# Kernel tuning notes

Hardware: AMD Instinct MI355X
Metric: run time of the kernel (lower is better)

Reference implementation:

```python
import jax, jax.numpy as jnp
import numpy as np

MAX_Z = 54  # atomic numbers up to iodine (53)
_mv = np.full(MAX_Z, 4.0, np.float32)
for z, v in {6: 4, 7: 3, 8: 2, 16: 6, 9: 1, 17: 1, 35: 1, 53: 1, 15: 5, 1: 1}.items():
    _mv[z] = v
_vdw = np.full(MAX_Z, 1.6, np.float32)  # default_radius = 1.6
for z, r in {1: 1.2, 6: 1.7, 7: 1.55, 8: 1.52, 9: 1.47, 15: 1.8, 16: 1.8, 17: 1.75, 35: 1.85, 53: 1.98}.items():
    _vdw[z] = r
_bl = np.full((MAX_Z, MAX_Z), 1.5, np.float32)  # default_length = 1.5
for (a, b), L in {(6, 6): 1.54, (6, 7): 1.47, (6, 8): 1.43, (6, 16): 1.82, (6, 9): 1.35, (6, 17): 1.77, (6, 1): 1.09, (7, 7): 1.45, (7, 8): 1.40, (7, 1): 1.01, (8, 8): 1.48, (8, 1): 0.96, (16, 16): 2.05, (15, 8): 1.63}.items():
    _bl[a, b] = L
    _bl[b, a] = L  # symmetric == tuple(sorted(...)) lookup
MAX_VAL = jnp.asarray(_mv)
VDW = jnp.asarray(_vdw)
BOND = jnp.asarray(_bl)
BIG = 1e9  # stands in for torch's float('inf') diagonal mask


def _forward(pos, edge_index, atom_types):
    N = pos.shape[0]
    row, col = edge_index[0], edge_index[1]
    # --- valence violations: scatter-add out-degree per atom ---
    bond_counts = jnp.zeros((N,), pos.dtype).at[row].add(1.0)
    violation = jnp.maximum(bond_counts - MAX_VAL[atom_types], 0.0)  # >0 iff counts > max_val
    loss = jnp.sum(violation ** 2)
    # Sequential valence push. Original loops atoms in ascending order and each atom's
    # neighbors in edge-list order; a stable sort of edges by row reproduces exactly that
    # visitation order, so a scan over sorted edges matches the sequential semantics
    # (pos_new[i] updates feed later direction computations).
    order = jnp.argsort(row)  # jnp.argsort is stable
    rs, cs = row[order], col[order]

    def step(p, rc):
        r, c = rc
        v = violation[r]
        d = p[r] - p[c]
        dist = jnp.linalg.norm(d) + 1e-8
        return p.at[r].add(jnp.where(v > 0, d / dist * v * 1e-3, 0.0)), None

    pos_new, _ = jax.lax.scan(step, pos, (rs, cs))
    # --- bond-length correction (gather per edge, scatter back per atom) ---
    bond_vec = pos_new[row] - pos_new[col]                        # [E,3]
    cur_len = jnp.linalg.norm(bond_vec, axis=-1, keepdims=True)   # [E,1]
    tgt_len = BOND[atom_types[row], atom_types[col]][:, None]     # [E,1]
    loss = loss + jnp.mean(jnp.abs(cur_len - tgt_len) ** 2)
    ratio = jnp.clip(tgt_len / (cur_len + 1e-8), 0.98, 1.02)
    adj = (bond_vec * ratio - bond_vec) * 0.01
    pos_new = pos_new + jnp.zeros_like(pos).at[row].add(adj * 0.5).at[col].add(-adj * 0.5)
    # --- steric clash repulsion over all atom pairs (cdist) ---
    sq = jnp.sum(pos_new ** 2, axis=-1)
    d2 = sq[:, None] + sq[None, :] - 2.0 * (pos_new @ pos_new.T)  # [N,N]
    eye = jnp.eye(N, dtype=bool)
    dist = jnp.sqrt(jnp.maximum(jnp.where(eye, 1.0, d2), 1e-20))
    dist = jnp.where(eye, BIG, dist)  # diagonal masked to +inf in the original
    rad = VDW[atom_types]
    min_d = (rad[:, None] + rad[None, :]) * 0.8
    loss = loss + jnp.sum(jax.nn.relu(min_d - dist) ** 2) / 2.0
    # original loops unordered clash pairs i<j updating i and j symmetrically; the full
    # symmetric double sum below is mathematically identical and avoids an [N,N,3] tensor:
    mask = (dist < min_d) & (dist > 1e-8)
    coeff = jnp.where(mask, (min_d - dist) * 0.005 * 0.5 / dist, 0.0)  # [N,N]
    steric = coeff.sum(axis=1)[:, None] * pos_new - coeff @ pos_new    # sum_j c_ij (p_i - p_j)
    return pos_new + steric, loss * 0.1


def setup_inputs() -> dict:
    key = jax.random.key(0)
    k1, k2, k3, k4 = jax.random.split(key, 4)
    N, E = 8192, 32768
    pos = jax.random.normal(k1, (N, 3), jnp.float32) * 6.0  # coords in an ~Angstrom-scale blob
    elements = jnp.array([1, 6, 7, 8, 9, 15, 16, 17], jnp.int32)  # H C N O F P S Cl
    atom_types = elements[jax.random.randint(k2, (N,), 0, 8)]
    edge_index = jnp.stack([jax.random.randint(k3, (E,), 0, N),
                            jax.random.randint(k4, (E,), 0, N)]).astype(jnp.int32)
    return {"pos": pos, "edge_index": edge_index, "atom_types": atom_types}


def reference(pos, edge_index, atom_types):
    return _forward(pos, edge_index, atom_types)
```

## Files before the change

kernel.cpp:

```cpp
#include <hip/hip_runtime.h>
#include <math.h>

#define NA 8192
#define NE 32768
#define NT 256
#define JSPLIT 32
#define JCHUNK (NA / JSPLIT)
#define NIB 16

#define WS_DEG      0
#define WS_LOSS     (WS_DEG + NA)
#define WS_DD       (WS_LOSS + 4)
#define WS_ZERO_END (WS_DD + 3*NA)
#define WS_PART     ((WS_ZERO_END + 3) & ~3)

__device__ __forceinline__ float maxval_of(int z) {
    switch (z) {
        case 1: return 1.f; case 6: return 4.f; case 7: return 3.f; case 8: return 2.f;
        case 9: return 1.f; case 15: return 5.f; case 16: return 6.f; case 17: return 1.f;
        case 35: return 1.f; case 53: return 1.f; default: return 4.f;
    }
}
__device__ __forceinline__ float vdw_of(int z) {
    switch (z) {
        case 1: return 1.2f; case 6: return 1.7f; case 7: return 1.55f; case 8: return 1.52f;
        case 9: return 1.47f; case 15: return 1.8f; case 16: return 1.8f; case 17: return 1.75f;
        case 35: return 1.85f; case 53: return 1.98f; default: return 1.6f;
    }
}
__device__ __forceinline__ float bond_of(int a, int b) {
    int lo = a < b ? a : b, hi = a < b ? b : a;
    switch (lo * 64 + hi) {
        case 6*64+6:   return 1.54f;
        case 6*64+7:   return 1.47f;
        case 6*64+8:   return 1.43f;
        case 6*64+16:  return 1.82f;
        case 6*64+9:   return 1.35f;
        case 6*64+17:  return 1.77f;
        case 1*64+6:   return 1.09f;
        case 7*64+7:   return 1.45f;
        case 7*64+8:   return 1.40f;
        case 1*64+7:   return 1.01f;
        case 8*64+8:   return 1.48f;
        case 1*64+8:   return 0.96f;
        case 16*64+16: return 2.05f;
        case 8*64+15:  return 1.63f;
        default:       return 1.5f;
    }
}
__device__ __forceinline__ float viol_of(int d, int z) {
    return fmaxf((float)d - maxval_of(z), 0.f);
}

__device__ __forceinline__ float wave_reduce_sum(float x) {
    #pragma unroll
    for (int off = 32; off > 0; off >>= 1) x += __shfl_down(x, off);
    return x;
}

__global__ void k_deg(const int* __restrict__ row, int* __restrict__ deg) {
    int e = blockIdx.x * NT + threadIdx.x;
    if (e < NE) atomicAdd(&deg[row[e]], 1);
}

__global__ void k_edge(const int* __restrict__ row, const int* __restrict__ col,
                       const int* __restrict__ types, const int* __restrict__ deg,
                       const float* __restrict__ pos, float* __restrict__ dD,
                       float* __restrict__ lossAcc) {
    int e = blockIdx.x * NT + threadIdx.x;
    float l1 = 0.f, l0 = 0.f;
    if (e < NE) {
        int r = row[e], c = col[e];
        float bx = pos[3*r]   - pos[3*c];
        float by = pos[3*r+1] - pos[3*c+1];
        float bz = pos[3*r+2] - pos[3*c+2];
        float cur = sqrtf(bx*bx + by*by + bz*bz);
        float tgt = bond_of(types[r], types[c]);
        float diff = cur - tgt;
        l1 = diff * diff;
        float ratio = tgt / (cur + 1e-8f);
        ratio = fminf(fmaxf(ratio, 0.98f), 1.02f);
        float s = (ratio - 1.f) * 0.01f * 0.5f;
        float v = viol_of(deg[r], types[r]);
        float sc = (v > 0.f) ? (v * 1e-3f / (cur + 1e-8f)) : 0.f;
        float rs = s + sc;
        atomicAdd(&dD[3*r],   bx * rs);
        atomicAdd(&dD[3*r+1], by * rs);
        atomicAdd(&dD[3*r+2], bz * rs);
        atomicAdd(&dD[3*c],   -bx * s);
        atomicAdd(&dD[3*c+1], -by * s);
        atomicAdd(&dD[3*c+2], -bz * s);
    }
    if (e < NA) {
        float v = viol_of(deg[e], types[e]);
        l0 = v * v;
    }
    float p1 = wave_reduce_sum(l1);
    float p0 = wave_reduce_sum(l0);
    if ((threadIdx.x & 63) == 0) {
        if (p1 != 0.f) atomicAdd(&lossAcc[1], p1);
        if (p0 != 0.f) atomicAdd(&lossAcc[0], p0);
    }
}

__device__ __forceinline__ void steric_pair(const float4 p, const float4 q,
                                            float& cs, float& sx, float& sy, float& sz,
                                            float& ll) {
    float dx = p.x - q.x, dy = p.y - q.y, dz = p.z - q.z;
    float d2 = fmaf(dx, dx, fmaf(dy, dy, dz * dz));
    float md = p.w + q.w;
    float rinv = rsqrtf(fmaxf(d2, 1e-12f));
    float dist = d2 * rinv;
    float t1 = md - dist;
    bool ok = (t1 > 0.f) && (d2 > 1e-12f);
    float t1c = ok ? t1 : 0.f;
    ll = fmaf(t1c, t1c, ll);
    float co = t1c * rinv;
    cs += co;
    sx = fmaf(co, q.x, sx);
    sy = fmaf(co, q.y, sy);
    sz = fmaf(co, q.z, sz);
}

__global__ void __launch_bounds__(NT)
k_steric(const float* __restrict__ pos, const float* __restrict__ dD,
         const int* __restrict__ types, float4* __restrict__ partial,
         float* __restrict__ lossAcc) {
    __shared__ float4 sm[JCHUNK];
    const int t = threadIdx.x;
    const int b = blockIdx.x;
    const int yb = b >> 4;
    const int ib = b & 15;
    int j = yb * JCHUNK + t;
    sm[t] = make_float4(pos[3*j]   + dD[3*j],
                        pos[3*j+1] + dD[3*j+1],
                        pos[3*j+2] + dD[3*j+2],
                        vdw_of(types[j]) * 0.8f);
    const int i0 = ib * 512 + t;
    const int i1 = i0 + 256;
    float4 p0 = make_float4(pos[3*i0] + dD[3*i0], pos[3*i0+1] + dD[3*i0+1],
                            pos[3*i0+2] + dD[3*i0+2], vdw_of(types[i0]) * 0.8f);
    float4 p1 = make_float4(pos[3*i1] + dD[3*i1], pos[3*i1+1] + dD[3*i1+1],
                            pos[3*i1+2] + dD[3*i1+2], vdw_of(types[i1]) * 0.8f);
    __syncthreads();
    float cs0 = 0.f, sx0 = 0.f, sy0 = 0.f, sz0 = 0.f;
    float cs1 = 0.f, sx1 = 0.f, sy1 = 0.f, sz1 = 0.f;
    float ll = 0.f;
    #pragma unroll 8
    for (int jj = 0; jj < JCHUNK; jj++) {
        float4 q = sm[jj];
        steric_pair(p0, q, cs0, sx0, sy0, sz0, ll);
        steric_pair(p1, q, cs1, sx1, sy1, sz1, ll);
    }
    partial[yb * NA + i0] = make_float4(cs0, sx0, sy0, sz0);
    partial[yb * NA + i1] = make_float4(cs1, sx1, sy1, sz1);
    float part = wave_reduce_sum(ll);
    if ((t & 63) == 0 && part != 0.f) atomicAdd(&lossAcc[2], part);
}

__global__ void k_reduce(const float* __restrict__ pos, const float* __restrict__ dD,
                         const float4* __restrict__ partial,
                         const float* __restrict__ lossAcc, float* __restrict__ out) {
    int a = blockIdx.x * NT + threadIdx.x;
    float cs = 0.f, sx = 0.f, sy = 0.f, sz = 0.f;
    #pragma unroll 8
    for (int y = 0; y < JSPLIT; y++) {
        float4 u = partial[y * NA + a];
        cs += u.x; sx += u.y; sy += u.z; sz += u.w;
    }
    float px = pos[3*a]   + dD[3*a];
    float py = pos[3*a+1] + dD[3*a+1];
    float pz = pos[3*a+2] + dD[3*a+2];
    float c = 1.f + cs * 0.0025f;
    out[3*a]   = px * c - sx * 0.0025f;
    out[3*a+1] = py * c - sy * 0.0025f;
    out[3*a+2] = pz * c - sz * 0.0025f;
    if (a == 0) {
        float loss = lossAcc[0] + lossAcc[1] * (1.f / NE) + lossAcc[2] * 0.5f;
        out[3*NA] = loss * 0.1f;
    }
}

extern "C" void kernel_launch(void* const* d_in, const int* in_sizes, int n_in,
                              void* d_out, int out_size, void* d_ws, size_t ws_size,
                              hipStream_t stream) {
    (void)in_sizes; (void)n_in; (void)out_size; (void)ws_size;
    const float* pos   = (const float*)d_in[0];
    const int*   eidx  = (const int*)d_in[1];
    const int*   types = (const int*)d_in[2];
    const int* row = eidx;
    const int* col = eidx + NE;

    int*   ws_i = (int*)d_ws;
    float* ws_f = (float*)d_ws;
    int*    deg     = ws_i + WS_DEG;
    float*  lossAcc = ws_f + WS_LOSS;
    float*  dD      = ws_f + WS_DD;
    float4* partial = (float4*)(ws_f + WS_PART);
    float*  out     = (float*)d_out;

    hipMemsetAsync(d_ws, 0, (size_t)WS_ZERO_END * 4, stream);
    k_deg   <<<NE/NT, NT, 0, stream>>>(row, deg);
    k_edge  <<<NE/NT, NT, 0, stream>>>(row, col, types, deg, pos, dD, lossAcc);
    k_steric<<<JSPLIT*NIB, NT, 0, stream>>>(pos, dD, types, partial, lossAcc);
    k_reduce<<<NA/NT, NT, 0, stream>>>(pos, dD, partial, lossAcc, out);
}
```

Measured before the change: 130.1 us.

## Accumulate steric displacement directly and double the j-split for more blocks

The steric pair now accumulates co*(p_i - p_j) directly, which removes the separate coefficient-sum accumulator and one add per pair, and the final reduce becomes a single FMA per component. The j-dimension split rises from 32 to 64 chunks when the workspace is large enough, giving 1024 blocks of shorter loops to fill more compute units. The cost is twice the partial-sum traffic in the reduce kernel. The clamp logic is also simplified with fmaxf.

```diff
diff --git a/kernel.cpp b/kernel.cpp
--- a/kernel.cpp
+++ b/kernel.cpp
@@ -4,9 +4,6 @@
 #define NA 8192
 #define NE 32768
 #define NT 256
-#define JSPLIT 32
-#define JCHUNK (NA / JSPLIT)
-#define NIB 16
 
 #define WS_DEG      0
 #define WS_LOSS     (WS_DEG + NA)
@@ -104,77 +101,80 @@
 }
 
 __device__ __forceinline__ void steric_pair(const float4 p, const float4 q,
-                                            float& cs, float& sx, float& sy, float& sz,
+                                            float& sx, float& sy, float& sz,
                                             float& ll) {
     float dx = p.x - q.x, dy = p.y - q.y, dz = p.z - q.z;
     float d2 = fmaf(dx, dx, fmaf(dy, dy, dz * dz));
     float md = p.w + q.w;
     float rinv = rsqrtf(fmaxf(d2, 1e-12f));
     float dist = d2 * rinv;
-    float t1 = md - dist;
-    bool ok = (t1 > 0.f) && (d2 > 1e-12f);
-    float t1c = ok ? t1 : 0.f;
+    float t1 = fmaxf(md - dist, 0.f);
+    float t1c = (d2 > 1e-12f) ? t1 : 0.f;
     ll = fmaf(t1c, t1c, ll);
     float co = t1c * rinv;
-    cs += co;
-    sx = fmaf(co, q.x, sx);
-    sy = fmaf(co, q.y, sy);
-    sz = fmaf(co, q.z, sz);
-}
-
+    sx = fmaf(co, dx, sx);
+    sy = fmaf(co, dy, sy);
+    sz = fmaf(co, dz, sz);
+}
+
+template<int JSPLIT>
 __global__ void __launch_bounds__(NT)
 k_steric(const float* __restrict__ pos, const float* __restrict__ dD,
          const int* __restrict__ types, float4* __restrict__ partial,
          float* __restrict__ lossAcc) {
+    constexpr int JCHUNK = NA / JSPLIT;
+    constexpr int NIB    = NA / (NT * 2);
     __shared__ float4 sm[JCHUNK];
     const int t = threadIdx.x;
     const int b = blockIdx.x;
-    const int yb = b >> 4;
-    const int ib = b & 15;
-    int j = yb * JCHUNK + t;
-    sm[t] = make_float4(pos[3*j]   + dD[3*j],
-                        pos[3*j+1] + dD[3*j+1],
-                        pos[3*j+2] + dD[3*j+2],
-                        vdw_of(types[j]) * 0.8f);
-    const int i0 = ib * 512 + t;
-    const int i1 = i0 + 256;
+    const int yb = b / NIB;
+    const int ib = b % NIB;
+    if (t < JCHUNK) {
+        int j = yb * JCHUNK + t;
+        sm[t] = make_float4(pos[3*j]   + dD[3*j],
+                            pos[3*j+1] + dD[3*j+1],
+                            pos[3*j+2] + dD[3*j+2],
+                            vdw_of(types[j]) * 0.8f);
+    }
+    const int i0 = ib * (NT * 2) + t;
+    const int i1 = i0 + NT;
     float4 p0 = make_float4(pos[3*i0] + dD[3*i0], pos[3*i0+1] + dD[3*i0+1],
                             pos[3*i0+2] + dD[3*i0+2], vdw_of(types[i0]) * 0.8f);
     float4 p1 = make_float4(pos[3*i1] + dD[3*i1], pos[3*i1+1] + dD[3*i1+1],
                             pos[3*i1+2] + dD[3*i1+2], vdw_of(types[i1]) * 0.8f);
     __syncthreads();
-    float cs0 = 0.f, sx0 = 0.f, sy0 = 0.f, sz0 = 0.f;
-    float cs1 = 0.f, sx1 = 0.f, sy1 = 0.f, sz1 = 0.f;
+    float sx0 = 0.f, sy0 = 0.f, sz0 = 0.f;
+    float sx1 = 0.f, sy1 = 0.f, sz1 = 0.f;
     float ll = 0.f;
     #pragma unroll 8
     for (int jj = 0; jj < JCHUNK; jj++) {
         float4 q = sm[jj];
-        steric_pair(p0, q, cs0, sx0, sy0, sz0, ll);
-        steric_pair(p1, q, cs1, sx1, sy1, sz1, ll);
-    }
-    partial[yb * NA + i0] = make_float4(cs0, sx0, sy0, sz0);
-    partial[yb * NA + i1] = make_float4(cs1, sx1, sy1, sz1);
+        steric_pair(p0, q, sx0, sy0, sz0, ll);
+        steric_pair(p1, q, sx1, sy1, sz1, ll);
+    }
+    partial[yb * NA + i0] = make_float4(sx0, sy0, sz0, 0.f);
+    partial[yb * NA + i1] = make_float4(sx1, sy1, sz1, 0.f);
     float part = wave_reduce_sum(ll);
     if ((t & 63) == 0 && part != 0.f) atomicAdd(&lossAcc[2], part);
 }
 
+template<int JSPLIT>
 __global__ void k_reduce(const float* __restrict__ pos, const float* __restrict__ dD,
                          const float4* __restrict__ partial,
                          const float* __restrict__ lossAcc, float* __restrict__ out) {
     int a = blockIdx.x * NT + threadIdx.x;
-    float cs = 0.f, sx = 0.f, sy = 0.f, sz = 0.f;
+    float sx = 0.f, sy = 0.f, sz = 0.f;
     #pragma unroll 8
     for (int y = 0; y < JSPLIT; y++) {
         float4 u = partial[y * NA + a];
-        cs += u.x; sx += u.y; sy += u.z; sz += u.w;
+        sx += u.x; sy += u.y; sz += u.z;
     }
     float px = pos[3*a]   + dD[3*a];
     float py = pos[3*a+1] + dD[3*a+1];
     float pz = pos[3*a+2] + dD[3*a+2];
-    float c = 1.f + cs * 0.0025f;
-    out[3*a]   = px * c - sx * 0.0025f;
-    out[3*a+1] = py * c - sy * 0.0025f;
-    out[3*a+2] = pz * c - sz * 0.0025f;
+    out[3*a]   = fmaf(sx, 0.0025f, px);
+    out[3*a+1] = fmaf(sy, 0.0025f, py);
+    out[3*a+2] = fmaf(sz, 0.0025f, pz);
     if (a == 0) {
         float loss = lossAcc[0] + lossAcc[1] * (1.f / NE) + lossAcc[2] * 0.5f;
         out[3*NA] = loss * 0.1f;
@@ -184,7 +184,7 @@
 extern "C" void kernel_launch(void* const* d_in, const int* in_sizes, int n_in,
                               void* d_out, int out_size, void* d_ws, size_t ws_size,
                               hipStream_t stream) {
-    (void)in_sizes; (void)n_in; (void)out_size; (void)ws_size;
+    (void)in_sizes; (void)n_in; (void)out_size;
     const float* pos   = (const float*)d_in[0];
     const int*   eidx  = (const int*)d_in[1];
     const int*   types = (const int*)d_in[2];
@@ -202,6 +202,14 @@
     hipMemsetAsync(d_ws, 0, (size_t)WS_ZERO_END * 4, stream);
     k_deg   <<<NE/NT, NT, 0, stream>>>(row, deg);
     k_edge  <<<NE/NT, NT, 0, stream>>>(row, col, types, deg, pos, dD, lossAcc);
-    k_steric<<<JSPLIT*NIB, NT, 0, stream>>>(pos, dD, types, partial, lossAcc);
-    k_reduce<<<NA/NT, NT, 0, stream>>>(pos, dD, partial, lossAcc, out);
-}
+
+    const size_t need64 = (size_t)WS_PART * 4 + (size_t)64 * NA * sizeof(float4);
+    constexpr int NIB = NA / (NT * 2);
+    if (ws_size == 0 || ws_size >= need64) {
+        k_steric<64><<<64 * NIB, NT, 0, stream>>>(pos, dD, types, partial, lossAcc);
+        k_reduce<64><<<NA/NT, NT, 0, stream>>>(pos, dD, partial, lossAcc, out);
+    } else {
+        k_steric<32><<<32 * NIB, NT, 0, stream>>>(pos, dD, types, partial, lossAcc);
+        k_reduce<32><<<NA/NT, NT, 0, stream>>>(pos, dD, partial, lossAcc, out);
+    }
+}
```

Measured after the change: 151.1 us. +16.1%, slower.

## Fuse all stages into one cooperative kernel with grid-wide syncs

Applied to the files above, without the earlier changes.

Replaces the memset plus four separate kernel launches with a single cooperative kernel of 512 blocks that zeroes the workspace, counts degrees, applies edge corrections, computes steric partials and reduces them, separated by grid.sync() barriers. The aim is to remove per-launch overhead and the gaps between kernels. In exchange it adds grid-wide barrier cost, requires all 512 blocks to be co-resident, and the edge and zeroing phases now run on the same 512x256 threads as the steric phase.

```diff
diff --git a/kernel.cpp b/kernel.cpp
--- a/kernel.cpp
+++ b/kernel.cpp
@@ -1,9 +1,13 @@
 #include <hip/hip_runtime.h>
+#include <hip/hip_cooperative_groups.h>
 #include <math.h>
+
+namespace cg = cooperative_groups;
 
 #define NA 8192
 #define NE 32768
 #define NT 256
+#define NB 512
 #define JSPLIT 32
 #define JCHUNK (NA / JSPLIT)
 #define NIB 16
@@ -58,51 +62,6 @@
     return x;
 }
 
-__global__ void k_deg(const int* __restrict__ row, int* __restrict__ deg) {
-    int e = blockIdx.x * NT + threadIdx.x;
-    if (e < NE) atomicAdd(&deg[row[e]], 1);
-}
-
-__global__ void k_edge(const int* __restrict__ row, const int* __restrict__ col,
-                       const int* __restrict__ types, const int* __restrict__ deg,
-                       const float* __restrict__ pos, float* __restrict__ dD,
-                       float* __restrict__ lossAcc) {
-    int e = blockIdx.x * NT + threadIdx.x;
-    float l1 = 0.f, l0 = 0.f;
-    if (e < NE) {
-        int r = row[e], c = col[e];
-        float bx = pos[3*r]   - pos[3*c];
-        float by = pos[3*r+1] - pos[3*c+1];
-        float bz = pos[3*r+2] - pos[3*c+2];
-        float cur = sqrtf(bx*bx + by*by + bz*bz);
-        float tgt = bond_of(types[r], types[c]);
-        float diff = cur - tgt;
-        l1 = diff * diff;
-        float ratio = tgt / (cur + 1e-8f);
-        ratio = fminf(fmaxf(ratio, 0.98f), 1.02f);
-        float s = (ratio - 1.f) * 0.01f * 0.5f;
-        float v = viol_of(deg[r], types[r]);
-        float sc = (v > 0.f) ? (v * 1e-3f / (cur + 1e-8f)) : 0.f;
-        float rs = s + sc;
-        atomicAdd(&dD[3*r],   bx * rs);
-        atomicAdd(&dD[3*r+1], by * rs);
-        atomicAdd(&dD[3*r+2], bz * rs);
-        atomicAdd(&dD[3*c],   -bx * s);
-        atomicAdd(&dD[3*c+1], -by * s);
-        atomicAdd(&dD[3*c+2], -bz * s);
-    }
-    if (e < NA) {
-        float v = viol_of(deg[e], types[e]);
-        l0 = v * v;
-    }
-    float p1 = wave_reduce_sum(l1);
-    float p0 = wave_reduce_sum(l0);
-    if ((threadIdx.x & 63) == 0) {
-        if (p1 != 0.f) atomicAdd(&lossAcc[1], p1);
-        if (p0 != 0.f) atomicAdd(&lossAcc[0], p0);
-    }
-}
-
 __device__ __forceinline__ void steric_pair(const float4 p, const float4 q,
                                             float& cs, float& sx, float& sy, float& sz,
                                             float& ll) {
@@ -123,61 +82,116 @@
 }
 
 __global__ void __launch_bounds__(NT)
-k_steric(const float* __restrict__ pos, const float* __restrict__ dD,
-         const int* __restrict__ types, float4* __restrict__ partial,
-         float* __restrict__ lossAcc) {
-    __shared__ float4 sm[JCHUNK];
-    const int t = threadIdx.x;
-    const int b = blockIdx.x;
-    const int yb = b >> 4;
-    const int ib = b & 15;
-    int j = yb * JCHUNK + t;
-    sm[t] = make_float4(pos[3*j]   + dD[3*j],
-                        pos[3*j+1] + dD[3*j+1],
-                        pos[3*j+2] + dD[3*j+2],
-                        vdw_of(types[j]) * 0.8f);
-    const int i0 = ib * 512 + t;
-    const int i1 = i0 + 256;
-    float4 p0 = make_float4(pos[3*i0] + dD[3*i0], pos[3*i0+1] + dD[3*i0+1],
-                            pos[3*i0+2] + dD[3*i0+2], vdw_of(types[i0]) * 0.8f);
-    float4 p1 = make_float4(pos[3*i1] + dD[3*i1], pos[3*i1+1] + dD[3*i1+1],
-                            pos[3*i1+2] + dD[3*i1+2], vdw_of(types[i1]) * 0.8f);
-    __syncthreads();
-    float cs0 = 0.f, sx0 = 0.f, sy0 = 0.f, sz0 = 0.f;
-    float cs1 = 0.f, sx1 = 0.f, sy1 = 0.f, sz1 = 0.f;
-    float ll = 0.f;
-    #pragma unroll 8
-    for (int jj = 0; jj < JCHUNK; jj++) {
-        float4 q = sm[jj];
-        steric_pair(p0, q, cs0, sx0, sy0, sz0, ll);
-        steric_pair(p1, q, cs1, sx1, sy1, sz1, ll);
-    }
-    partial[yb * NA + i0] = make_float4(cs0, sx0, sy0, sz0);
-    partial[yb * NA + i1] = make_float4(cs1, sx1, sy1, sz1);
-    float part = wave_reduce_sum(ll);
-    if ((t & 63) == 0 && part != 0.f) atomicAdd(&lossAcc[2], part);
-}
-
-__global__ void k_reduce(const float* __restrict__ pos, const float* __restrict__ dD,
-                         const float4* __restrict__ partial,
-                         const float* __restrict__ lossAcc, float* __restrict__ out) {
-    int a = blockIdx.x * NT + threadIdx.x;
-    float cs = 0.f, sx = 0.f, sy = 0.f, sz = 0.f;
-    #pragma unroll 8
-    for (int y = 0; y < JSPLIT; y++) {
-        float4 u = partial[y * NA + a];
-        cs += u.x; sx += u.y; sy += u.z; sz += u.w;
-    }
-    float px = pos[3*a]   + dD[3*a];
-    float py = pos[3*a+1] + dD[3*a+1];
-    float pz = pos[3*a+2] + dD[3*a+2];
-    float c = 1.f + cs * 0.0025f;
-    out[3*a]   = px * c - sx * 0.0025f;
-    out[3*a+1] = py * c - sy * 0.0025f;
-    out[3*a+2] = pz * c - sz * 0.0025f;
-    if (a == 0) {
-        float loss = lossAcc[0] + lossAcc[1] * (1.f / NE) + lossAcc[2] * 0.5f;
-        out[3*NA] = loss * 0.1f;
+k_mega(const float* __restrict__ pos, const int* __restrict__ eidx,
+       const int* __restrict__ types, int* __restrict__ ws,
+       float* __restrict__ out) {
+    cg::grid_group grid = cg::this_grid();
+    const int* row = eidx;
+    const int* col = eidx + NE;
+    int*    deg     = ws + WS_DEG;
+    float*  wsf     = (float*)ws;
+    float*  lossAcc = wsf + WS_LOSS;
+    float*  dD      = wsf + WS_DD;
+    float4* partial = (float4*)(wsf + WS_PART);
+
+    const int t   = threadIdx.x;
+    const int b   = blockIdx.x;
+    const int tid = b * NT + t;
+
+    if (tid < WS_ZERO_END) ws[tid] = 0;
+    grid.sync();
+
+    if (tid < NE) atomicAdd(&deg[row[tid]], 1);
+    grid.sync();
+
+    {
+        float l1 = 0.f, l0 = 0.f;
+        if (tid < NE) {
+            int r = row[tid], c = col[tid];
+            float bx = pos[3*r]   - pos[3*c];
+            float by = pos[3*r+1] - pos[3*c+1];
+            float bz = pos[3*r+2] - pos[3*c+2];
+            float cur = sqrtf(bx*bx + by*by + bz*bz);
+            float tgt = bond_of(types[r], types[c]);
+            float diff = cur - tgt;
+            l1 = diff * diff;
+            float ratio = tgt / (cur + 1e-8f);
+            ratio = fminf(fmaxf(ratio, 0.98f), 1.02f);
+            float s = (ratio - 1.f) * 0.01f * 0.5f;
+            float v = viol_of(deg[r], types[r]);
+            float sc = (v > 0.f) ? (v * 1e-3f / (cur + 1e-8f)) : 0.f;
+            float rs = s + sc;
+            atomicAdd(&dD[3*r],   bx * rs);
+            atomicAdd(&dD[3*r+1], by * rs);
+            atomicAdd(&dD[3*r+2], bz * rs);
+            atomicAdd(&dD[3*c],   -bx * s);
+            atomicAdd(&dD[3*c+1], -by * s);
+            atomicAdd(&dD[3*c+2], -bz * s);
+        }
+        if (tid < NA) {
+            float v = viol_of(deg[tid], types[tid]);
+            l0 = v * v;
+        }
+        float p1 = wave_reduce_sum(l1);
+        float p0 = wave_reduce_sum(l0);
+        if ((t & 63) == 0) {
+            if (p1 != 0.f) atomicAdd(&lossAcc[1], p1);
+            if (p0 != 0.f) atomicAdd(&lossAcc[0], p0);
+        }
+    }
+    grid.sync();
+
+    {
+        __shared__ float4 sm[JCHUNK];
+        const int yb = b >> 4;
+        const int ib = b & 15;
+        int j = yb * JCHUNK + t;
+        sm[t] = make_float4(pos[3*j]   + dD[3*j],
+                            pos[3*j+1] + dD[3*j+1],
+                            pos[3*j+2] + dD[3*j+2],
+                            vdw_of(types[j]) * 0.8f);
+        const int i0 = ib * 512 + t;
+        const int i1 = i0 + 256;
+        float4 p0 = make_float4(pos[3*i0] + dD[3*i0], pos[3*i0+1] + dD[3*i0+1],
+                                pos[3*i0+2] + dD[3*i0+2], vdw_of(types[i0]) * 0.8f);
+        float4 p1 = make_float4(pos[3*i1] + dD[3*i1], pos[3*i1+1] + dD[3*i1+1],
+                                pos[3*i1+2] + dD[3*i1+2], vdw_of(types[i1]) * 0.8f);
+        __syncthreads();
+        float cs0 = 0.f, sx0 = 0.f, sy0 = 0.f, sz0 = 0.f;
+        float cs1 = 0.f, sx1 = 0.f, sy1 = 0.f, sz1 = 0.f;
+        float ll = 0.f;
+        #pragma unroll 8
+        for (int jj = 0; jj < JCHUNK; jj++) {
+            float4 q = sm[jj];
+            steric_pair(p0, q, cs0, sx0, sy0, sz0, ll);
+            steric_pair(p1, q, cs1, sx1, sy1, sz1, ll);
+        }
+        partial[yb * NA + i0] = make_float4(cs0, sx0, sy0, sz0);
+        partial[yb * NA + i1] = make_float4(cs1, sx1, sy1, sz1);
+        float part = wave_reduce_sum(ll);
+        if ((t & 63) == 0 && part != 0.f) atomicAdd(&lossAcc[2], part);
+    }
+    grid.sync();
+
+    if (tid < NA) {
+        int a = tid;
+        float cs = 0.f, sx = 0.f, sy = 0.f, sz = 0.f;
+        #pragma unroll 8
+        for (int y = 0; y < JSPLIT; y++) {
+            float4 u = partial[y * NA + a];
+            cs += u.x; sx += u.y; sy += u.z; sz += u.w;
+        }
+        float px = pos[3*a]   + dD[3*a];
+        float py = pos[3*a+1] + dD[3*a+1];
+        float pz = pos[3*a+2] + dD[3*a+2];
+        float c = 1.f + cs * 0.0025f;
+        out[3*a]   = px * c - sx * 0.0025f;
+        out[3*a+1] = py * c - sy * 0.0025f;
+        out[3*a+2] = pz * c - sz * 0.0025f;
+        if (a == 0) {
+            float loss = lossAcc[0] + lossAcc[1] * (1.f / NE) + lossAcc[2] * 0.5f;
+            out[3*NA] = loss * 0.1f;
+        }
     }
 }
 
@@ -188,20 +202,11 @@
     const float* pos   = (const float*)d_in[0];
     const int*   eidx  = (const int*)d_in[1];
     const int*   types = (const int*)d_in[2];
-    const int* row = eidx;
-    const int* col = eidx + NE;
-
-    int*   ws_i = (int*)d_ws;
-    float* ws_f = (float*)d_ws;
-    int*    deg     = ws_i + WS_DEG;
-    float*  lossAcc = ws_f + WS_LOSS;
-    float*  dD      = ws_f + WS_DD;
-    float4* partial = (float4*)(ws_f + WS_PART);
-    float*  out     = (float*)d_out;
-
-    hipMemsetAsync(d_ws, 0, (size_t)WS_ZERO_END * 4, stream);
-    k_deg   <<<NE/NT, NT, 0, stream>>>(row, deg);
-    k_edge  <<<NE/NT, NT, 0, stream>>>(row, col, types, deg, pos, dD, lossAcc);
-    k_steric<<<JSPLIT*NIB, NT, 0, stream>>>(pos, dD, types, partial, lossAcc);
-    k_reduce<<<NA/NT, NT, 0, stream>>>(pos, dD, partial, lossAcc, out);
-}
+    int*         ws    = (int*)d_ws;
+    float*       out   = (float*)d_out;
+
+    void* args[] = { (void*)&pos, (void*)&eidx, (void*)&types,
+                     (void*)&ws, (void*)&out };
+    hipLaunchCooperativeKernel((const void*)k_mega, dim3(NB), dim3(NT),
+                               args, 0, stream);
+}
```

Result: slower. 316.2 us (+143.0%).
